# Performance work log

Measured on AMD Instinct MI355X. Metric: run time of the kernel, lower is better.

Reference implementation:

```python
import jax, jax.numpy as jnp
import numpy as np

EPS = 1e-5
B, C, T = 128, 64, 1000          # batch, EEG channels, time samples
NCLU, HID, NOUT = 8, 512, 4      # clusters, head hidden dim, outputs (=feature_dim)


def _conv1d(x, w):
    # x: (N, Cin, T), w: (Cout, Cin, K), valid conv along time
    return jax.lax.conv_general_dilated(x, w, (1,), 'VALID',
                                        dimension_numbers=('NCH', 'OIH', 'NCH'))


def _bn(x, g, b, m, v):
    # eval-mode BatchNorm over channel dim of (N, C, T)
    return (x - m[None, :, None]) * (g / jnp.sqrt(v + EPS))[None, :, None] + b[None, :, None]


def _pool3(x):
    # maxpool kernel 3 stride 3 along time
    return jax.lax.reduce_window(x, -jnp.inf, jax.lax.max, (1, 1, 3), (1, 1, 3), 'VALID')


def setup_inputs() -> dict:
    key = jax.random.key(0)
    ks = jax.random.split(key, 12)
    def nrm(k, shape, fan):
        return jax.random.normal(k, shape, jnp.float32) / np.float32(np.sqrt(fan))
    inp = {
        'x': jax.random.normal(ks[0], (B, C, T), jnp.float32),
        'cluster_ids': jax.random.randint(ks[1], (B,), 0, NCLU, jnp.int32),
        # Deep4Net-style backbone params
        'w_time': nrm(ks[2], (25, 1, 10), 10),
        'b_time': jnp.zeros((25,), jnp.float32),
        'w_spat': nrm(ks[3], (25, 25, C), 25 * C),
        'w2': nrm(ks[4], (50, 25, 10), 250),
        'w3': nrm(ks[5], (100, 50, 10), 500),
        'w4': nrm(ks[6], (200, 100, 10), 1000),
        'w_cls': nrm(ks[7], (NOUT, 200, 7), 1400),
        'b_cls': jnp.zeros((NOUT,), jnp.float32),
        # per-cluster expert head params
        'hW1': nrm(ks[8], (NCLU, HID, NOUT), NOUT),
        'hb1': jnp.zeros((NCLU, HID), jnp.float32),
        'hW2': nrm(ks[9], (NCLU, NOUT, HID), HID),
        'hb2': jnp.zeros((NCLU, NOUT), jnp.float32),
        'hg': jnp.ones((NCLU, HID), jnp.float32),
        'hbe': jnp.zeros((NCLU, HID), jnp.float32),
        'hm': jnp.zeros((NCLU, HID), jnp.float32),
        'hv': jnp.ones((NCLU, HID), jnp.float32),
    }
    for i, c in zip((1, 2, 3, 4), (25, 50, 100, 200)):
        inp[f'g{i}'] = jnp.ones((c,), jnp.float32)
        inp[f'be{i}'] = jnp.zeros((c,), jnp.float32)
        inp[f'm{i}'] = jnp.zeros((c,), jnp.float32)
        inp[f'v{i}'] = jnp.ones((c,), jnp.float32)
    return inp


def reference(x, cluster_ids, w_time, b_time, w_spat, w2, w3, w4, w_cls, b_cls,
              hW1, hb1, hW2, hb2, hg, hbe, hm, hv,
              g1, be1, m1, v1, g2, be2, m2, v2, g3, be3, m3, v3, g4, be4, m4, v4):
    b_, c_, t_ = x.shape
    # conv_time: same 25 temporal filters applied per EEG channel -> (B, C, 25, T1)
    h = _conv1d(x.reshape(b_ * c_, 1, t_), w_time) + b_time[None, :, None]
    h = h.reshape(b_, c_, 25, -1)
    # conv_spat: collapse EEG channel axis -> (B, 25, T1)
    z = jnp.einsum('bcft,gfc->bgt', h, w_spat)
    z = _pool3(jax.nn.elu(_bn(z, g1, be1, m1, v1)))
    for w, g, be, m, v in ((w2, g2, be2, m2, v2), (w3, g3, be3, m3, v3), (w4, g4, be4, m4, v4)):
        z = _pool3(jax.nn.elu(_bn(_conv1d(z, w), g, be, m, v)))
    # final_conv_length='auto': classifier conv reduces time dim to 1 -> (B, NOUT)
    feats = (_conv1d(z, w_cls) + b_cls[None, :, None])[:, :, 0]
    # per-sample expert head routing (Linear -> BN(eval) -> ReLU -> [Dropout eval] -> Linear)
    h1 = jnp.einsum('bf,bhf->bh', feats, hW1[cluster_ids]) + hb1[cluster_ids]
    h1 = (h1 - hm[cluster_ids]) * (hg[cluster_ids] / jnp.sqrt(hv[cluster_ids] + EPS)) + hbe[cluster_ids]
    h1 = jax.nn.relu(h1)
    return jnp.einsum('bh,boh->bo', h1, hW2[cluster_ids]) + hb2[cluster_ids]
```

## Files before the change

### kernel.cpp

```cpp
#include <hip/hip_runtime.h>
#include <math.h>

#define EPS_BN 1e-5f

typedef __attribute__((ext_vector_type(8))) short short8;
typedef __attribute__((ext_vector_type(4))) float f32x4;
typedef __attribute__((ext_vector_type(4))) unsigned int uint4v;

__device__ __forceinline__ unsigned short f2bf(float f) {
    unsigned int u = __float_as_uint(f);
    u = (u + 0x7fffu + ((u >> 16) & 1u)) >> 16;
    return (unsigned short)u;
}
__device__ __forceinline__ float bf2f(unsigned short s) {
    return __uint_as_float(((unsigned int)s) << 16);
}
__device__ __forceinline__ float elu1(float y) { return y > 0.f ? y : expm1f(y); }
__device__ __forceinline__ float warp_sum(float v) {
    for (int off = 32; off > 0; off >>= 1) v += __shfl_down(v, off);
    return v;
}

#define UW1 0
#define UW2 20480
#define UW3 40960
#define UW4 122880
#define BB1 0
#define BB2 32
#define BB3 96
#define BB4 224
#define XTG_U 410496
#define Z1G_U 9192320
#define Z2G_U 10544000
#define Z3G_U 11420544
#define Z4G_BYTE 24372992

#define NPREP 1602
#define RS_ZB 36

__global__ __launch_bounds__(256) void kprep_tr(
    const float* __restrict__ x,
    const float* __restrict__ w_time, const float* __restrict__ b_time,
    const float* __restrict__ w_spat,
    const float* __restrict__ w2, const float* __restrict__ w3,
    const float* __restrict__ w4,
    const float* __restrict__ g1, const float* __restrict__ be1,
    const float* __restrict__ m1, const float* __restrict__ v1,
    const float* __restrict__ g2, const float* __restrict__ be2,
    const float* __restrict__ m2, const float* __restrict__ v2,
    const float* __restrict__ g3, const float* __restrict__ be3,
    const float* __restrict__ m3, const float* __restrict__ v3,
    const float* __restrict__ g4, const float* __restrict__ be4,
    const float* __restrict__ m4, const float* __restrict__ v4,
    unsigned short* __restrict__ wsz, float* __restrict__ biasf) {
    __shared__ float tr[64 * 65];
    if (blockIdx.x < NPREP) {
        int idx = blockIdx.x * 256 + threadIdx.x;
        if (idx < 20480) {
            int k = idx >> 11, g = (idx >> 6) & 31, c = idx & 63;
            float val = 0.f;
            if (g < 25) {
                float s = 0.f;
#pragma unroll
                for (int f = 0; f < 25; ++f)
                    s = fmaf(w_spat[g * 1600 + f * 64 + c], w_time[f * 10 + k], s);
                val = s * (g1[g] * rsqrtf(v1[g] + EPS_BN));
            }
            wsz[UW1 + idx] = f2bf(val);
        } else if (idx < 40960) {
            int j = idx - 20480;
            int k = j >> 11, g = (j >> 5) & 63, c = j & 31;
            float val = 0.f;
            if (g < 50 && c < 25)
                val = w2[(g * 25 + c) * 10 + k] * (g2[g] * rsqrtf(v2[g] + EPS_BN));
            wsz[UW2 + j] = f2bf(val);
        } else if (idx < 122880) {
            int j = idx - 40960;
            int k = j >> 13, g = (j >> 6) & 127, c = j & 63;
            float val = 0.f;
            if (g < 100 && c < 50)
                val = w3[(g * 50 + c) * 10 + k] * (g3[g] * rsqrtf(v3[g] + EPS_BN));
            wsz[UW3 + j] = f2bf(val);
        } else if (idx < 409600) {
            int j = idx - 122880;
            int k = j / 28672, r = j % 28672, g = r >> 7, c = r & 127;
            float val = 0.f;
            if (g < 200 && c < 100)
                val = w4[(g * 100 + c) * 10 + k] * (g4[g] * rsqrtf(v4[g] + EPS_BN));
            wsz[UW4 + j] = f2bf(val);
        } else if (idx < 410048) {
            int j = idx - 409600;
            if (j < 32) {
                int g = j; float val = 0.f;
                if (g < 25) {
                    float beff = 0.f;
                    for (int f = 0; f < 25; ++f) {
                        float a = 0.f;
                        for (int c = 0; c < 64; ++c) a += w_spat[g * 1600 + f * 64 + c];
                        beff = fmaf(a, b_time[f], beff);
                    }
                    float sc = g1[g] * rsqrtf(v1[g] + EPS_BN);
                    val = be1[g] - m1[g] * sc + beff * sc;
                }
                biasf[BB1 + g] = val;
            } else if (j < 96) {
                int g = j - 32; float val = 0.f;
                if (g < 50) { float sc = g2[g] * rsqrtf(v2[g] + EPS_BN); val = be2[g] - m2[g] * sc; }
                biasf[BB2 + g] = val;
            } else if (j < 224) {
                int g = j - 96; float val = 0.f;
                if (g < 100) { float sc = g3[g] * rsqrtf(v3[g] + EPS_BN); val = be3[g] - m3[g] * sc; }
                biasf[BB3 + g] = val;
            } else {
                int g = j - 224; float val = 0.f;
                if (g < 200) { float sc = g4[g] * rsqrtf(v4[g] + EPS_BN); val = be4[g] - m4[g] * sc; }
                biasf[BB4 + g] = val;
            }
        }
    } else {
        const int bid = blockIdx.x - NPREP;
        const int b = bid / 17, tile = bid % 17, t = threadIdx.x;
        const int t0 = tile * 64;
        const float* xb = x + b * 64000;
        for (int idx = t; idx < 1024; idx += 256) {
            int c = idx >> 4, q = idx & 15;
            int tg = t0 + 4 * q;
            float4 v = {0.f, 0.f, 0.f, 0.f};
            if (tg + 4 <= 1000) {
                v = *(const float4*)(xb + c * 1000 + tg);
            } else {
                float* pv = (float*)&v;
#pragma unroll
                for (int e = 0; e < 4; ++e)
                    if (tg + e < 1000) pv[e] = xb[c * 1000 + tg + e];
            }
            tr[c * 65 + 4 * q]     = v.x;
            tr[c * 65 + 4 * q + 1] = v.y;
            tr[c * 65 + 4 * q + 2] = v.z;
            tr[c * 65 + 4 * q + 3] = v.w;
        }
        __syncthreads();
        unsigned short* xTg = wsz + XTG_U;
        for (int idx = t; idx < 2048; idx += 256) {
            int tl = idx >> 5, cp = idx & 31;
            int tg = t0 + tl;
            unsigned int pk = 0u;
            if (tg < 1000)
                pk = (unsigned int)f2bf(tr[(2 * cp) * 65 + tl]) |
                     ((unsigned int)f2bf(tr[(2 * cp + 1) * 65 + tl]) << 16);
            if (tg < 1072)
                *(unsigned int*)&xTg[(b * 1072 + tg) * 64 + 2 * cp] = pk;
        }
    }
}

template<int CPAD, int RS, int SP, int TT, int TPC, int NCHUNK, int JMAX,
         int NTCH, int GPAD, int TPOOL, int GSTORE, int NGV, int OUT_RS,
         bool OUT_F32, int NW, int KPRE>
__device__ __forceinline__ void conv_core(
    const unsigned short* xT, const unsigned short* __restrict__ wpk,
    const float* __restrict__ bias,
    unsigned short* zout, float* zoutf, unsigned short* zb,
    int t, int jbeg, int jend, int t0b) {
    const int lane = t & 63;
    const int wv = __builtin_amdgcn_readfirstlane(t >> 6);
    const int lm = lane & 15, h8 = lane >> 4;
    const int gloc = lane & 31, hh = lane >> 5;
    unsigned short* zbw = zb + wv * (48 * RS_ZB);

    for (int job = jbeg + wv; job < jend; job += NW) {
        const int gbi = job / NTCH, tci = job % NTCH;
        const int tl0 = tci * (TT * 16) - t0b;
        const int po0 = tci * (NCHUNK * 16);

        f32x4 acc[TT][2];
#pragma unroll
        for (int i = 0; i < TT; ++i) {
            acc[i][0] = (f32x4){0.f, 0.f, 0.f, 0.f};
            acc[i][1] = (f32x4){0.f, 0.f, 0.f, 0.f};
        }

        const int abase = (tl0 + lm) * RS + h8 * 8;
        const unsigned short* wp = wpk + (gbi * 32 + lm) * CPAD + h8 * 8;
#pragma unroll
        for (int ph = 0; ph < 10 / KPRE; ++ph) {
            short8 w0r[KPRE][SP], w1r[KPRE][SP];
#pragma unroll
            for (int kk = 0; kk < KPRE; ++kk) {
                const int k = ph * KPRE + kk;
#pragma unroll
                for (int s = 0; s < SP; ++s) {
                    w0r[kk][s] = *(const short8*)(wp + k * (GPAD * CPAD) + s * 32);
                    w1r[kk][s] = *(const short8*)(wp + k * (GPAD * CPAD) + 16 * CPAD + s * 32);
                }
            }
#pragma unroll
            for (int kk = 0; kk < KPRE; ++kk) {
                const int k = ph * KPRE + kk;
#pragma unroll
                for (int s = 0; s < SP; ++s) {
#pragma unroll
                    for (int tt = 0; tt < TT; ++tt) {
                        short8 a = *(const short8*)&xT[abase + (tt * 16 + k) * RS + s * 32];
                        acc[tt][0] = __builtin_amdgcn_mfma_f32_16x16x32_bf16(
                            a, w0r[kk][s], acc[tt][0], 0, 0, 0);
                        acc[tt][1] = __builtin_amdgcn_mfma_f32_16x16x32_bf16(
                            a, w1r[kk][s], acc[tt][1], 0, 0, 0);
                    }
                }
            }
        }

        const float bv0 = bias[gbi * 32 + lm];
        const float bv1 = bias[gbi * 32 + 16 + lm];
#pragma unroll
        for (int ch = 0; ch < NCHUNK; ++ch) {
#pragma unroll
            for (int ti = 0; ti < TPC; ++ti) {
                int ttg = ch * TPC + ti;
#pragma unroll
                for (int r = 0; r < 4; ++r) {
                    float v0 = elu1(acc[ttg][0][r] + bv0);
                    float v1 = elu1(acc[ttg][1][r] + bv1);
                    int row = ti * 16 + 4 * h8 + r;
                    zbw[row * RS_ZB + lm] = f2bf(v0);
                    zbw[row * RS_ZB + 16 + lm] = f2bf(v1);
                }
            }
#pragma unroll
            for (int j = 0; j < JMAX; ++j) {
                int po = hh + 2 * j;
                if (3 * po + 2 < TPC * 16) {
                    float q0 = bf2f(zbw[(3 * po) * RS_ZB + gloc]);
                    float q1 = bf2f(zbw[(3 * po + 1) * RS_ZB + gloc]);
                    float q2 = bf2f(zbw[(3 * po + 2) * RS_ZB + gloc]);
                    float mx = fmaxf(q0, fmaxf(q1, q2));
                    int poa = po0 + ch * 16 + po;
                    int ga = gbi * 32 + gloc;
                    if (poa < TPOOL && ga < GSTORE) {
                        if constexpr (OUT_F32)
                            zoutf[poa * OUT_RS + ga] = mx;
                        else
                            zout[poa * OUT_RS + ga] =
                                (ga < NGV) ? f2bf(mx) : (unsigned short)0;
                    }
                }
            }
        }
    }
}

__global__ __launch_bounds__(64) void ks1(
    const unsigned short* __restrict__ wsu, const float* __restrict__ biasf,
    unsigned short* __restrict__ wsz) {
    __shared__ __align__(16) unsigned short xT[64 * 72];
    __shared__ __align__(16) unsigned short zb[48 * RS_ZB];
    const int b = blockIdx.x, tci = blockIdx.y, t = threadIdx.x;
    const int t0b = tci * 48;
    const unsigned short* xTg = wsz + XTG_U + (b * 1072 + t0b) * 64;
    for (int idx = t; idx < 64 * 8; idx += 64) {
        int r = idx >> 3, q = idx & 7;
        *(uint4v*)&xT[r * 72 + 8 * q] = *(const uint4v*)&xTg[r * 64 + 8 * q];
    }
    __syncthreads();
    conv_core<64, 72, 2, 3, 3, 1, 8, 21, 32, 330, 32, 25, 32, false, 1, 5>(
        xT, wsu + UW1, biasf + BB1, wsz + Z1G_U + b * 330 * 32, nullptr, zb,
        t, tci, tci + 1, t0b);
}

__global__ __launch_bounds__(64) void ks2(
    const unsigned short* __restrict__ wsu, const float* __restrict__ biasf,
    unsigned short* __restrict__ wsz) {
    __shared__ __align__(16) unsigned short xT[64 * 40];
    __shared__ __align__(16) unsigned short zb[48 * RS_ZB];
    const int b = blockIdx.x, job = blockIdx.y, t = threadIdx.x;
    const int t0b = (job % 7) * 48;
    const unsigned short* z1g = wsz + Z1G_U + b * 330 * 32;
    for (int idx = t; idx < 64 * 4; idx += 64) {
        int r = idx >> 2, q = idx & 3;
        uint4v v = {0u, 0u, 0u, 0u};
        if (t0b + r < 330) v = *(const uint4v*)&z1g[(t0b + r) * 32 + 8 * q];
        *(uint4v*)&xT[r * 40 + 8 * q] = v;
    }
    __syncthreads();
    conv_core<32, 40, 1, 3, 3, 1, 8, 7, 64, 107, 64, 50, 64, false, 1, 5>(
        xT, wsu + UW2, biasf + BB2, wsz + Z2G_U + b * 107 * 64, nullptr, zb,
        t, job, job + 1, t0b);
}

__global__ __launch_bounds__(64) void ks3(
    const unsigned short* __restrict__ wsu, const float* __restrict__ biasf,
    unsigned short* __restrict__ wsz) {
    __shared__ __align__(16) unsigned short z2t[64 * 72];
    __shared__ __align__(16) unsigned short zb[48 * RS_ZB];
    const int b = blockIdx.x, job = blockIdx.y, t = threadIdx.x;
    const int t0b = (job % 2) * 48;
    const unsigned short* z2g = wsz + Z2G_U + b * 107 * 64;
    for (int idx = t; idx < 64 * 8; idx += 64) {
        int r = idx >> 3, q = idx & 7;
        uint4v v = {0u, 0u, 0u, 0u};
        if (t0b + r < 107) v = *(const uint4v*)&z2g[(t0b + r) * 64 + 8 * q];
        *(uint4v*)&z2t[r * 72 + 8 * q] = v;
    }
    __syncthreads();
    conv_core<64, 72, 2, 3, 3, 1, 8, 2, 128, 32, 128, 100, 136, false, 1, 5>(
        z2t, wsu + UW3, biasf + BB3, wsz + Z3G_U + b * 44 * 136, nullptr, zb,
        t, job, job + 1, t0b);
}

__global__ __launch_bounds__(64) void ks4(
    const unsigned short* __restrict__ wsu, const float* __restrict__ biasf,
    unsigned short* __restrict__ wsz, float* __restrict__ z4g) {
    __shared__ __align__(16) unsigned short z3t[44 * 136];
    __shared__ __align__(16) unsigned short zb[48 * RS_ZB];
    const int b = blockIdx.x, gbi = blockIdx.y, t = threadIdx.x;
    const unsigned short* z3g = wsz + Z3G_U + b * 44 * 136;
    for (int idx = t; idx < 44 * 17; idx += 64) {
        int r = idx / 17, q = idx % 17;
        uint4v v = {0u, 0u, 0u, 0u};
        if (r < 32) v = *(const uint4v*)&z3g[r * 136 + 8 * q];
        *(uint4v*)&z3t[r * 136 + 8 * q] = v;
    }
    __syncthreads();
    conv_core<128, 136, 4, 2, 2, 1, 4, 1, 224, 7, 200, 200, 200, true, 1, 5>(
        z3t, wsu + UW4, biasf + BB4, nullptr, z4g + b * 1400, zb,
        t, gbi, gbi + 1, 0);
}

__global__ __launch_bounds__(256) void kh(
    const float* __restrict__ z4g,
    const float* __restrict__ w_cls, const float* __restrict__ b_cls,
    const int* __restrict__ cid,
    const float* __restrict__ hW1, const float* __restrict__ hb1,
    const float* __restrict__ hW2, const float* __restrict__ hb2,
    const float* __restrict__ hg, const float* __restrict__ hbe,
    const float* __restrict__ hm, const float* __restrict__ hv,
    float* __restrict__ out) {
    __shared__ float z4f[1400];
    __shared__ float feats[4];
    __shared__ float h1s[512];
    const int b = blockIdx.x, t = threadIdx.x;
    for (int i = t; i < 1400; i += 256) z4f[i] = z4g[b * 1400 + i];
    __syncthreads();

    const int wv = t >> 6, lane = t & 63;
    {
        float p = 0.f;
        for (int i = lane; i < 1400; i += 64) {
            int po = i / 200, g = i - po * 200;
            p = fmaf(z4f[i], w_cls[wv * 1400 + g * 7 + po], p);
        }
        p = warp_sum(p);
        if (lane == 0) feats[wv] = p + b_cls[wv];
    }
    __syncthreads();

    const int c = cid[b];
    const float f0 = feats[0], f1 = feats[1], f2 = feats[2], f3 = feats[3];
    for (int h = t; h < 512; h += 256) {
        const float* w1 = &hW1[(c * 512 + h) * 4];
        float v = f0 * w1[0] + f1 * w1[1] + f2 * w1[2] + f3 * w1[3] + hb1[c * 512 + h];
        float sc = hg[c * 512 + h] * rsqrtf(hv[c * 512 + h] + EPS_BN);
        v = (v - hm[c * 512 + h]) * sc + hbe[c * 512 + h];
        h1s[h] = fmaxf(v, 0.f);
    }
    __syncthreads();
    {
        float p = 0.f;
        for (int i = lane; i < 512; i += 64)
            p = fmaf(h1s[i], hW2[(c * 4 + wv) * 512 + i], p);
        p = warp_sum(p);
        if (lane == 0) out[b * 4 + wv] = p + hb2[c * 4 + wv];
    }
}

extern "C" void kernel_launch(void* const* d_in, const int* in_sizes, int n_in,
                              void* d_out, int out_size, void* d_ws, size_t ws_size,
                              hipStream_t stream) {
    const float* x      = (const float*)d_in[0];
    const int*   cid    = (const int*)d_in[1];
    const float* w_time = (const float*)d_in[2];
    const float* b_time = (const float*)d_in[3];
    const float* w_spat = (const float*)d_in[4];
    const float* w2     = (const float*)d_in[5];
    const float* w3     = (const float*)d_in[6];
    const float* w4     = (const float*)d_in[7];
    const float* w_cls  = (const float*)d_in[8];
    const float* b_cls  = (const float*)d_in[9];
    const float* hW1    = (const float*)d_in[10];
    const float* hb1    = (const float*)d_in[11];
    const float* hW2    = (const float*)d_in[12];
    const float* hb2    = (const float*)d_in[13];
    const float* hg     = (const float*)d_in[14];
    const float* hbe    = (const float*)d_in[15];
    const float* hm     = (const float*)d_in[16];
    const float* hv     = (const float*)d_in[17];
    const float* g1  = (const float*)d_in[18];
    const float* be1 = (const float*)d_in[19];
    const float* m1  = (const float*)d_in[20];
    const float* v1  = (const float*)d_in[21];
    const float* g2  = (const float*)d_in[22];
    const float* be2 = (const float*)d_in[23];
    const float* m2  = (const float*)d_in[24];
    const float* v2  = (const float*)d_in[25];
    const float* g3  = (const float*)d_in[26];
    const float* be3 = (const float*)d_in[27];
    const float* m3  = (const float*)d_in[28];
    const float* v3  = (const float*)d_in[29];
    const float* g4  = (const float*)d_in[30];
    const float* be4 = (const float*)d_in[31];
    const float* m4  = (const float*)d_in[32];
    const float* v4  = (const float*)d_in[33];

    unsigned short* wsz = (unsigned short*)d_ws;
    float* biasf = (float*)((char*)d_ws + 819200);
    float* z4g   = (float*)((char*)d_ws + Z4G_BYTE);
    float* out = (float*)d_out;

    kprep_tr<<<NPREP + 128 * 17, 256, 0, stream>>>(
        x, w_time, b_time, w_spat, w2, w3, w4,
        g1, be1, m1, v1, g2, be2, m2, v2, g3, be3, m3, v3, g4, be4, m4, v4,
        wsz, biasf);

    ks1<<<dim3(128, 21), 64, 0, stream>>>(wsz, biasf, wsz);
    ks2<<<dim3(128, 14), 64, 0, stream>>>(wsz, biasf, wsz);
    ks3<<<dim3(128, 8), 64, 0, stream>>>(wsz, biasf, wsz);
    ks4<<<dim3(128, 7), 64, 0, stream>>>(wsz, biasf, wsz, z4g);
    kh<<<128, 256, 0, stream>>>(z4g, w_cls, b_cls, cid, hW1, hb1, hW2, hb2,
                                hg, hbe, hm, hv, out);
}
```

Baseline: 102.4 us.

## Fuse all conv stages into one persistent cooperative kernel with grid syncs

Replaces the six separate kernel launches (prep/transpose, four conv stages, head) with a single cooperative kernel of 256 blocks × 8 waves that walks each stage as a wave-level job loop separated by grid-wide barriers. Each wave stages its own input tile in a private LDS slice and uses a waitcnt fence instead of block barriers. The aim is to remove launch gaps and tail effects between the small stages. In exchange it adds grid-sync cost and fixes the parallelism at 2048 waves, which may leave some stages under-occupied or unevenly loaded.

```diff
diff --git a/kernel.cpp b/kernel.cpp
--- a/kernel.cpp
+++ b/kernel.cpp
@@ -1,5 +1,8 @@
 #include <hip/hip_runtime.h>
+#include <hip/hip_cooperative_groups.h>
 #include <math.h>
+
+namespace cg = cooperative_groups;
 
 #define EPS_BN 1e-5f
 
@@ -19,6 +22,10 @@
 __device__ __forceinline__ float warp_sum(float v) {
     for (int off = 32; off > 0; off >>= 1) v += __shfl_down(v, off);
     return v;
+}
+__device__ __forceinline__ void lds_fence() {
+    asm volatile("s_waitcnt lgkmcnt(0)" ::: "memory");
+    __builtin_amdgcn_sched_barrier(0);
 }
 
 #define UW1 0
@@ -35,27 +42,122 @@
 #define Z3G_U 11420544
 #define Z4G_BYTE 24372992
 
-#define NPREP 1602
 #define RS_ZB 36
-
-__global__ __launch_bounds__(256) void kprep_tr(
-    const float* __restrict__ x,
-    const float* __restrict__ w_time, const float* __restrict__ b_time,
-    const float* __restrict__ w_spat,
-    const float* __restrict__ w2, const float* __restrict__ w3,
-    const float* __restrict__ w4,
-    const float* __restrict__ g1, const float* __restrict__ be1,
-    const float* __restrict__ m1, const float* __restrict__ v1,
-    const float* __restrict__ g2, const float* __restrict__ be2,
-    const float* __restrict__ m2, const float* __restrict__ v2,
-    const float* __restrict__ g3, const float* __restrict__ be3,
-    const float* __restrict__ m3, const float* __restrict__ v3,
-    const float* __restrict__ g4, const float* __restrict__ be4,
-    const float* __restrict__ m4, const float* __restrict__ v4,
-    unsigned short* __restrict__ wsz, float* __restrict__ biasf) {
-    __shared__ float tr[64 * 65];
-    if (blockIdx.x < NPREP) {
-        int idx = blockIdx.x * 256 + threadIdx.x;
+#define NWAVES 2048
+#define WSCR 15424
+
+struct KParams {
+    const float* x; const int* cid;
+    const float* w_time; const float* b_time; const float* w_spat;
+    const float* w2; const float* w3; const float* w4;
+    const float* w_cls; const float* b_cls;
+    const float* hW1; const float* hb1; const float* hW2; const float* hb2;
+    const float* hg; const float* hbe; const float* hm; const float* hv;
+    const float* g1; const float* be1; const float* m1; const float* v1;
+    const float* g2; const float* be2; const float* m2; const float* v2;
+    const float* g3; const float* be3; const float* m3; const float* v3;
+    const float* g4; const float* be4; const float* m4; const float* v4;
+    unsigned short* wsz; float* biasf; float* z4g; float* out;
+};
+
+template<int CPAD, int RS, int SP, int TT, int TPC, int NCHUNK, int JMAX,
+         int GPAD, int TPOOL, int GSTORE, int NGV, int OUT_RS, bool OUT_F32,
+         int KPRE>
+__device__ __forceinline__ void conv_job(
+    const unsigned short* xT, const unsigned short* __restrict__ wpk,
+    const float* __restrict__ bias,
+    unsigned short* zout, float* zoutf, unsigned short* zbw,
+    int lane, int gbi, int po0) {
+    const int lm = lane & 15, h8 = lane >> 4;
+    const int gloc = lane & 31, hh = lane >> 5;
+
+    f32x4 acc[TT][2];
+#pragma unroll
+    for (int i = 0; i < TT; ++i) {
+        acc[i][0] = (f32x4){0.f, 0.f, 0.f, 0.f};
+        acc[i][1] = (f32x4){0.f, 0.f, 0.f, 0.f};
+    }
+
+    const int abase = lm * RS + h8 * 8;
+    const unsigned short* wp = wpk + (gbi * 32 + lm) * CPAD + h8 * 8;
+#pragma unroll
+    for (int ph = 0; ph < 10 / KPRE; ++ph) {
+        short8 w0r[KPRE][SP], w1r[KPRE][SP];
+#pragma unroll
+        for (int kk = 0; kk < KPRE; ++kk) {
+            const int k = ph * KPRE + kk;
+#pragma unroll
+            for (int s = 0; s < SP; ++s) {
+                w0r[kk][s] = *(const short8*)(wp + k * (GPAD * CPAD) + s * 32);
+                w1r[kk][s] = *(const short8*)(wp + k * (GPAD * CPAD) + 16 * CPAD + s * 32);
+            }
+        }
+#pragma unroll
+        for (int kk = 0; kk < KPRE; ++kk) {
+            const int k = ph * KPRE + kk;
+#pragma unroll
+            for (int s = 0; s < SP; ++s) {
+#pragma unroll
+                for (int tt = 0; tt < TT; ++tt) {
+                    short8 a = *(const short8*)&xT[abase + (tt * 16 + k) * RS + s * 32];
+                    acc[tt][0] = __builtin_amdgcn_mfma_f32_16x16x32_bf16(
+                        a, w0r[kk][s], acc[tt][0], 0, 0, 0);
+                    acc[tt][1] = __builtin_amdgcn_mfma_f32_16x16x32_bf16(
+                        a, w1r[kk][s], acc[tt][1], 0, 0, 0);
+                }
+            }
+        }
+    }
+
+    const float bv0 = bias[gbi * 32 + lm];
+    const float bv1 = bias[gbi * 32 + 16 + lm];
+#pragma unroll
+    for (int ch = 0; ch < NCHUNK; ++ch) {
+#pragma unroll
+        for (int ti = 0; ti < TPC; ++ti) {
+            int ttg = ch * TPC + ti;
+#pragma unroll
+            for (int r = 0; r < 4; ++r) {
+                float v0 = elu1(acc[ttg][0][r] + bv0);
+                float v1 = elu1(acc[ttg][1][r] + bv1);
+                int row = ti * 16 + 4 * h8 + r;
+                zbw[row * RS_ZB + lm] = f2bf(v0);
+                zbw[row * RS_ZB + 16 + lm] = f2bf(v1);
+            }
+        }
+#pragma unroll
+        for (int j = 0; j < JMAX; ++j) {
+            int po = hh + 2 * j;
+            if (3 * po + 2 < TPC * 16) {
+                float q0 = bf2f(zbw[(3 * po) * RS_ZB + gloc]);
+                float q1 = bf2f(zbw[(3 * po + 1) * RS_ZB + gloc]);
+                float q2 = bf2f(zbw[(3 * po + 2) * RS_ZB + gloc]);
+                float mx = fmaxf(q0, fmaxf(q1, q2));
+                int poa = po0 + ch * 16 + po;
+                int ga = gbi * 32 + gloc;
+                if (poa < TPOOL && ga < GSTORE) {
+                    if constexpr (OUT_F32)
+                        zoutf[poa * OUT_RS + ga] = mx;
+                    else
+                        zout[poa * OUT_RS + ga] =
+                            (ga < NGV) ? f2bf(mx) : (unsigned short)0;
+                }
+            }
+        }
+    }
+}
+
+__global__ __launch_bounds__(512, 2) void kfused(KParams P) {
+    __shared__ __align__(16) unsigned char smem[8 * WSCR];
+    const int t = threadIdx.x;
+    const int lane = t & 63;
+    const int wv = t >> 6;
+    const int W = blockIdx.x * 8 + wv;
+    unsigned short* tile = (unsigned short*)(smem + wv * WSCR);
+    unsigned short* zbw  = (unsigned short*)(smem + wv * WSCR + 11968);
+    cg::grid_group gg = cg::this_grid();
+
+    for (int idx = blockIdx.x * 512 + t; idx < 410048; idx += 131072) {
         if (idx < 20480) {
             int k = idx >> 11, g = (idx >> 6) & 31, c = idx & 63;
             float val = 0.f;
@@ -63,31 +165,31 @@
                 float s = 0.f;
 #pragma unroll
                 for (int f = 0; f < 25; ++f)
-                    s = fmaf(w_spat[g * 1600 + f * 64 + c], w_time[f * 10 + k], s);
-                val = s * (g1[g] * rsqrtf(v1[g] + EPS_BN));
-            }
-            wsz[UW1 + idx] = f2bf(val);
+                    s = fmaf(P.w_spat[g * 1600 + f * 64 + c], P.w_time[f * 10 + k], s);
+                val = s * (P.g1[g] * rsqrtf(P.v1[g] + EPS_BN));
+            }
+            P.wsz[UW1 + idx] = f2bf(val);
         } else if (idx < 40960) {
             int j = idx - 20480;
             int k = j >> 11, g = (j >> 5) & 63, c = j & 31;
             float val = 0.f;
             if (g < 50 && c < 25)
-                val = w2[(g * 25 + c) * 10 + k] * (g2[g] * rsqrtf(v2[g] + EPS_BN));
-            wsz[UW2 + j] = f2bf(val);
+                val = P.w2[(g * 25 + c) * 10 + k] * (P.g2[g] * rsqrtf(P.v2[g] + EPS_BN));
+            P.wsz[UW2 + j] = f2bf(val);
         } else if (idx < 122880) {
             int j = idx - 40960;
             int k = j >> 13, g = (j >> 6) & 127, c = j & 63;
             float val = 0.f;
             if (g < 100 && c < 50)
-                val = w3[(g * 50 + c) * 10 + k] * (g3[g] * rsqrtf(v3[g] + EPS_BN));
-            wsz[UW3 + j] = f2bf(val);
+                val = P.w3[(g * 50 + c) * 10 + k] * (P.g3[g] * rsqrtf(P.v3[g] + EPS_BN));
+            P.wsz[UW3 + j] = f2bf(val);
         } else if (idx < 409600) {
             int j = idx - 122880;
             int k = j / 28672, r = j % 28672, g = r >> 7, c = r & 127;
             float val = 0.f;
             if (g < 200 && c < 100)
-                val = w4[(g * 100 + c) * 10 + k] * (g4[g] * rsqrtf(v4[g] + EPS_BN));
-            wsz[UW4 + j] = f2bf(val);
+                val = P.w4[(g * 100 + c) * 10 + k] * (P.g4[g] * rsqrtf(P.v4[g] + EPS_BN));
+            P.wsz[UW4 + j] = f2bf(val);
         } else if (idx < 410048) {
             int j = idx - 409600;
             if (j < 32) {
@@ -96,336 +198,214 @@
                     float beff = 0.f;
                     for (int f = 0; f < 25; ++f) {
                         float a = 0.f;
-                        for (int c = 0; c < 64; ++c) a += w_spat[g * 1600 + f * 64 + c];
-                        beff = fmaf(a, b_time[f], beff);
+                        for (int c = 0; c < 64; ++c) a += P.w_spat[g * 1600 + f * 64 + c];
+                        beff = fmaf(a, P.b_time[f], beff);
                     }
-                    float sc = g1[g] * rsqrtf(v1[g] + EPS_BN);
-                    val = be1[g] - m1[g] * sc + beff * sc;
+                    float sc = P.g1[g] * rsqrtf(P.v1[g] + EPS_BN);
+                    val = P.be1[g] - P.m1[g] * sc + beff * sc;
                 }
-                biasf[BB1 + g] = val;
+                P.biasf[BB1 + g] = val;
             } else if (j < 96) {
                 int g = j - 32; float val = 0.f;
-                if (g < 50) { float sc = g2[g] * rsqrtf(v2[g] + EPS_BN); val = be2[g] - m2[g] * sc; }
-                biasf[BB2 + g] = val;
+                if (g < 50) { float sc = P.g2[g] * rsqrtf(P.v2[g] + EPS_BN); val = P.be2[g] - P.m2[g] * sc; }
+                P.biasf[BB2 + g] = val;
             } else if (j < 224) {
                 int g = j - 96; float val = 0.f;
-                if (g < 100) { float sc = g3[g] * rsqrtf(v3[g] + EPS_BN); val = be3[g] - m3[g] * sc; }
-                biasf[BB3 + g] = val;
+                if (g < 100) { float sc = P.g3[g] * rsqrtf(P.v3[g] + EPS_BN); val = P.be3[g] - P.m3[g] * sc; }
+                P.biasf[BB3 + g] = val;
             } else {
                 int g = j - 224; float val = 0.f;
-                if (g < 200) { float sc = g4[g] * rsqrtf(v4[g] + EPS_BN); val = be4[g] - m4[g] * sc; }
-                biasf[BB4 + g] = val;
-            }
-        }
-    } else {
-        const int bid = blockIdx.x - NPREP;
-        const int b = bid / 17, tile = bid % 17, t = threadIdx.x;
-        const int t0 = tile * 64;
-        const float* xb = x + b * 64000;
-        for (int idx = t; idx < 1024; idx += 256) {
-            int c = idx >> 4, q = idx & 15;
-            int tg = t0 + 4 * q;
-            float4 v = {0.f, 0.f, 0.f, 0.f};
-            if (tg + 4 <= 1000) {
-                v = *(const float4*)(xb + c * 1000 + tg);
-            } else {
-                float* pv = (float*)&v;
-#pragma unroll
-                for (int e = 0; e < 4; ++e)
-                    if (tg + e < 1000) pv[e] = xb[c * 1000 + tg + e];
-            }
-            tr[c * 65 + 4 * q]     = v.x;
-            tr[c * 65 + 4 * q + 1] = v.y;
-            tr[c * 65 + 4 * q + 2] = v.z;
-            tr[c * 65 + 4 * q + 3] = v.w;
-        }
+                if (g < 200) { float sc = P.g4[g] * rsqrtf(P.v4[g] + EPS_BN); val = P.be4[g] - P.m4[g] * sc; }
+                P.biasf[BB4 + g] = val;
+            }
+        }
+    }
+
+    {
+        float* tr = (float*)smem;
+        unsigned short* xTg = P.wsz + XTG_U;
+        for (int tid2 = blockIdx.x; tid2 < 2176; tid2 += 256) {
+            const int b = tid2 / 17, tilei = tid2 % 17;
+            const int t0 = tilei * 64;
+            const float* xb = P.x + b * 64000;
+            __syncthreads();
+            for (int idx = t; idx < 1024; idx += 512) {
+                int c = idx >> 4, q = idx & 15;
+                int tg = t0 + 4 * q;
+                float4 v = {0.f, 0.f, 0.f, 0.f};
+                if (tg + 4 <= 1000) {
+                    v = *(const float4*)(xb + c * 1000 + tg);
+                } else {
+                    float* pv = (float*)&v;
+#pragma unroll
+                    for (int e = 0; e < 4; ++e)
+                        if (tg + e < 1000) pv[e] = xb[c * 1000 + tg + e];
+                }
+                tr[c * 65 + 4 * q]     = v.x;
+                tr[c * 65 + 4 * q + 1] = v.y;
+                tr[c * 65 + 4 * q + 2] = v.z;
+                tr[c * 65 + 4 * q + 3] = v.w;
+            }
+            __syncthreads();
+            for (int idx = t; idx < 2048; idx += 512) {
+                int tl = idx >> 5, cp = idx & 31;
+                int tg = t0 + tl;
+                unsigned int pk = 0u;
+                if (tg < 1000)
+                    pk = (unsigned int)f2bf(tr[(2 * cp) * 65 + tl]) |
+                         ((unsigned int)f2bf(tr[(2 * cp + 1) * 65 + tl]) << 16);
+                if (tg < 1072)
+                    *(unsigned int*)&xTg[(b * 1072 + tg) * 64 + 2 * cp] = pk;
+            }
+        }
+    }
+    gg.sync();
+
+    for (int jid = W; jid < 2688; jid += NWAVES) {
+        const int b = jid / 21, tci = jid % 21;
+        const unsigned short* src = P.wsz + XTG_U + (b * 1072 + tci * 48) * 64;
+        for (int idx = lane; idx < 512; idx += 64) {
+            int r = idx >> 3, q = idx & 7;
+            *(uint4v*)&tile[r * 72 + 8 * q] = *(const uint4v*)&src[r * 64 + 8 * q];
+        }
+        lds_fence();
+        conv_job<64, 72, 2, 3, 3, 1, 8, 32, 330, 32, 25, 32, false, 5>(
+            tile, P.wsz + UW1, P.biasf + BB1,
+            P.wsz + Z1G_U + b * 330 * 32, nullptr, zbw, lane, 0, tci * 16);
+    }
+    gg.sync();
+
+    for (int jid = W; jid < 1792; jid += NWAVES) {
+        const int b = jid / 14, y = jid % 14;
+        const int gbi = y / 7, tci = y % 7, t0b = tci * 48;
+        const unsigned short* z1g = P.wsz + Z1G_U + b * 330 * 32;
+        for (int idx = lane; idx < 256; idx += 64) {
+            int r = idx >> 2, q = idx & 3;
+            uint4v v = {0u, 0u, 0u, 0u};
+            if (t0b + r < 330) v = *(const uint4v*)&z1g[(t0b + r) * 32 + 8 * q];
+            *(uint4v*)&tile[r * 40 + 8 * q] = v;
+        }
+        lds_fence();
+        conv_job<32, 40, 1, 3, 3, 1, 8, 64, 107, 64, 50, 64, false, 5>(
+            tile, P.wsz + UW2, P.biasf + BB2,
+            P.wsz + Z2G_U + b * 107 * 64, nullptr, zbw, lane, gbi, tci * 16);
+    }
+    gg.sync();
+
+    for (int jid = W; jid < 1024; jid += NWAVES) {
+        const int b = jid / 8, y = jid % 8;
+        const int gbi = y / 2, tci = y % 2, t0b = tci * 48;
+        const unsigned short* z2g = P.wsz + Z2G_U + b * 107 * 64;
+        for (int idx = lane; idx < 512; idx += 64) {
+            int r = idx >> 3, q = idx & 7;
+            uint4v v = {0u, 0u, 0u, 0u};
+            if (t0b + r < 107) v = *(const uint4v*)&z2g[(t0b + r) * 64 + 8 * q];
+            *(uint4v*)&tile[r * 72 + 8 * q] = v;
+        }
+        lds_fence();
+        conv_job<64, 72, 2, 3, 3, 1, 8, 128, 32, 128, 100, 136, false, 5>(
+            tile, P.wsz + UW3, P.biasf + BB3,
+            P.wsz + Z3G_U + b * 44 * 136, nullptr, zbw, lane, gbi, tci * 16);
+    }
+    gg.sync();
+
+    for (int jid = W; jid < 896; jid += NWAVES) {
+        const int b = jid / 7, gbi = jid % 7;
+        const unsigned short* z3g = P.wsz + Z3G_U + b * 44 * 136;
+        for (int idx = lane; idx < 748; idx += 64) {
+            int r = idx / 17, q = idx % 17;
+            uint4v v = {0u, 0u, 0u, 0u};
+            if (r < 32) v = *(const uint4v*)&z3g[r * 136 + 8 * q];
+            *(uint4v*)&tile[r * 136 + 8 * q] = v;
+        }
+        lds_fence();
+        conv_job<128, 136, 4, 2, 2, 1, 4, 224, 7, 200, 200, 200, true, 5>(
+            tile, P.wsz + UW4, P.biasf + BB4,
+            nullptr, P.z4g + b * 1400, zbw, lane, gbi, 0);
+    }
+    gg.sync();
+
+    if (blockIdx.x < 128) {
+        const int b = blockIdx.x;
+        float* z4f   = (float*)smem;
+        float* feats = (float*)(smem + 5600);
+        float* h1s   = (float*)(smem + 5616);
+        for (int i = t; i < 1400; i += 512) z4f[i] = P.z4g[b * 1400 + i];
         __syncthreads();
-        unsigned short* xTg = wsz + XTG_U;
-        for (int idx = t; idx < 2048; idx += 256) {
-            int tl = idx >> 5, cp = idx & 31;
-            int tg = t0 + tl;
-            unsigned int pk = 0u;
-            if (tg < 1000)
-                pk = (unsigned int)f2bf(tr[(2 * cp) * 65 + tl]) |
-                     ((unsigned int)f2bf(tr[(2 * cp + 1) * 65 + tl]) << 16);
-            if (tg < 1072)
-                *(unsigned int*)&xTg[(b * 1072 + tg) * 64 + 2 * cp] = pk;
-        }
-    }
-}
-
-template<int CPAD, int RS, int SP, int TT, int TPC, int NCHUNK, int JMAX,
-         int NTCH, int GPAD, int TPOOL, int GSTORE, int NGV, int OUT_RS,
-         bool OUT_F32, int NW, int KPRE>
-__device__ __forceinline__ void conv_core(
-    const unsigned short* xT, const unsigned short* __restrict__ wpk,
-    const float* __restrict__ bias,
-    unsigned short* zout, float* zoutf, unsigned short* zb,
-    int t, int jbeg, int jend, int t0b) {
-    const int lane = t & 63;
-    const int wv = __builtin_amdgcn_readfirstlane(t >> 6);
-    const int lm = lane & 15, h8 = lane >> 4;
-    const int gloc = lane & 31, hh = lane >> 5;
-    unsigned short* zbw = zb + wv * (48 * RS_ZB);
-
-    for (int job = jbeg + wv; job < jend; job += NW) {
-        const int gbi = job / NTCH, tci = job % NTCH;
-        const int tl0 = tci * (TT * 16) - t0b;
-        const int po0 = tci * (NCHUNK * 16);
-
-        f32x4 acc[TT][2];
-#pragma unroll
-        for (int i = 0; i < TT; ++i) {
-            acc[i][0] = (f32x4){0.f, 0.f, 0.f, 0.f};
-            acc[i][1] = (f32x4){0.f, 0.f, 0.f, 0.f};
-        }
-
-        const int abase = (tl0 + lm) * RS + h8 * 8;
-        const unsigned short* wp = wpk + (gbi * 32 + lm) * CPAD + h8 * 8;
-#pragma unroll
-        for (int ph = 0; ph < 10 / KPRE; ++ph) {
-            short8 w0r[KPRE][SP], w1r[KPRE][SP];
-#pragma unroll
-            for (int kk = 0; kk < KPRE; ++kk) {
-                const int k = ph * KPRE + kk;
-#pragma unroll
-                for (int s = 0; s < SP; ++s) {
-                    w0r[kk][s] = *(const short8*)(wp + k * (GPAD * CPAD) + s * 32);
-                    w1r[kk][s] = *(const short8*)(wp + k * (GPAD * CPAD) + 16 * CPAD + s * 32);
-                }
-            }
-#pragma unroll
-            for (int kk = 0; kk < KPRE; ++kk) {
-                const int k = ph * KPRE + kk;
-#pragma unroll
-                for (int s = 0; s < SP; ++s) {
-#pragma unroll
-                    for (int tt = 0; tt < TT; ++tt) {
-                        short8 a = *(const short8*)&xT[abase + (tt * 16 + k) * RS + s * 32];
-                        acc[tt][0] = __builtin_amdgcn_mfma_f32_16x16x32_bf16(
-                            a, w0r[kk][s], acc[tt][0], 0, 0, 0);
-                        acc[tt][1] = __builtin_amdgcn_mfma_f32_16x16x32_bf16(
-                            a, w1r[kk][s], acc[tt][1], 0, 0, 0);
-                    }
-                }
-            }
-        }
-
-        const float bv0 = bias[gbi * 32 + lm];
-        const float bv1 = bias[gbi * 32 + 16 + lm];
-#pragma unroll
-        for (int ch = 0; ch < NCHUNK; ++ch) {
-#pragma unroll
-            for (int ti = 0; ti < TPC; ++ti) {
-                int ttg = ch * TPC + ti;
-#pragma unroll
-                for (int r = 0; r < 4; ++r) {
-                    float v0 = elu1(acc[ttg][0][r] + bv0);
-                    float v1 = elu1(acc[ttg][1][r] + bv1);
-                    int row = ti * 16 + 4 * h8 + r;
-                    zbw[row * RS_ZB + lm] = f2bf(v0);
-                    zbw[row * RS_ZB + 16 + lm] = f2bf(v1);
-                }
-            }
-#pragma unroll
-            for (int j = 0; j < JMAX; ++j) {
-                int po = hh + 2 * j;
-                if (3 * po + 2 < TPC * 16) {
-                    float q0 = bf2f(zbw[(3 * po) * RS_ZB + gloc]);
-                    float q1 = bf2f(zbw[(3 * po + 1) * RS_ZB + gloc]);
-                    float q2 = bf2f(zbw[(3 * po + 2) * RS_ZB + gloc]);
-                    float mx = fmaxf(q0, fmaxf(q1, q2));
-                    int poa = po0 + ch * 16 + po;
-                    int ga = gbi * 32 + gloc;
-                    if (poa < TPOOL && ga < GSTORE) {
-                        if constexpr (OUT_F32)
-                            zoutf[poa * OUT_RS + ga] = mx;
-                        else
-                            zout[poa * OUT_RS + ga] =
-                                (ga < NGV) ? f2bf(mx) : (unsigned short)0;
-                    }
-                }
-            }
-        }
-    }
-}
-
-__global__ __launch_bounds__(64) void ks1(
-    const unsigned short* __restrict__ wsu, const float* __restrict__ biasf,
-    unsigned short* __restrict__ wsz) {
-    __shared__ __align__(16) unsigned short xT[64 * 72];
-    __shared__ __align__(16) unsigned short zb[48 * RS_ZB];
-    const int b = blockIdx.x, tci = blockIdx.y, t = threadIdx.x;
-    const int t0b = tci * 48;
-    const unsigned short* xTg = wsz + XTG_U + (b * 1072 + t0b) * 64;
-    for (int idx = t; idx < 64 * 8; idx += 64) {
-        int r = idx >> 3, q = idx & 7;
-        *(uint4v*)&xT[r * 72 + 8 * q] = *(const uint4v*)&xTg[r * 64 + 8 * q];
-    }
-    __syncthreads();
-    conv_core<64, 72, 2, 3, 3, 1, 8, 21, 32, 330, 32, 25, 32, false, 1, 5>(
-        xT, wsu + UW1, biasf + BB1, wsz + Z1G_U + b * 330 * 32, nullptr, zb,
-        t, tci, tci + 1, t0b);
-}
-
-__global__ __launch_bounds__(64) void ks2(
-    const unsigned short* __restrict__ wsu, const float* __restrict__ biasf,
-    unsigned short* __restrict__ wsz) {
-    __shared__ __align__(16) unsigned short xT[64 * 40];
-    __shared__ __align__(16) unsigned short zb[48 * RS_ZB];
-    const int b = blockIdx.x, job = blockIdx.y, t = threadIdx.x;
-    const int t0b = (job % 7) * 48;
-    const unsigned short* z1g = wsz + Z1G_U + b * 330 * 32;
-    for (int idx = t; idx < 64 * 4; idx += 64) {
-        int r = idx >> 2, q = idx & 3;
-        uint4v v = {0u, 0u, 0u, 0u};
-        if (t0b + r < 330) v = *(const uint4v*)&z1g[(t0b + r) * 32 + 8 * q];
-        *(uint4v*)&xT[r * 40 + 8 * q] = v;
-    }
-    __syncthreads();
-    conv_core<32, 40, 1, 3, 3, 1, 8, 7, 64, 107, 64, 50, 64, false, 1, 5>(
-        xT, wsu + UW2, biasf + BB2, wsz + Z2G_U + b * 107 * 64, nullptr, zb,
-        t, job, job + 1, t0b);
-}
-
-__global__ __launch_bounds__(64) void ks3(
-    const unsigned short* __restrict__ wsu, const float* __restrict__ biasf,
-    unsigned short* __restrict__ wsz) {
-    __shared__ __align__(16) unsigned short z2t[64 * 72];
-    __shared__ __align__(16) unsigned short zb[48 * RS_ZB];
-    const int b = blockIdx.x, job = blockIdx.y, t = threadIdx.x;
-    const int t0b = (job % 2) * 48;
-    const unsigned short* z2g = wsz + Z2G_U + b * 107 * 64;
-    for (int idx = t; idx < 64 * 8; idx += 64) {
-        int r = idx >> 3, q = idx & 7;
-        uint4v v = {0u, 0u, 0u, 0u};
-        if (t0b + r < 107) v = *(const uint4v*)&z2g[(t0b + r) * 64 + 8 * q];
-        *(uint4v*)&z2t[r * 72 + 8 * q] = v;
-    }
-    __syncthreads();
-    conv_core<64, 72, 2, 3, 3, 1, 8, 2, 128, 32, 128, 100, 136, false, 1, 5>(
-        z2t, wsu + UW3, biasf + BB3, wsz + Z3G_U + b * 44 * 136, nullptr, zb,
-        t, job, job + 1, t0b);
-}
-
-__global__ __launch_bounds__(64) void ks4(
-    const unsigned short* __restrict__ wsu, const float* __restrict__ biasf,
-    unsigned short* __restrict__ wsz, float* __restrict__ z4g) {
-    __shared__ __align__(16) unsigned short z3t[44 * 136];
-    __shared__ __align__(16) unsigned short zb[48 * RS_ZB];
-    const int b = blockIdx.x, gbi = blockIdx.y, t = threadIdx.x;
-    const unsigned short* z3g = wsz + Z3G_U + b * 44 * 136;
-    for (int idx = t; idx < 44 * 17; idx += 64) {
-        int r = idx / 17, q = idx % 17;
-        uint4v v = {0u, 0u, 0u, 0u};
-        if (r < 32) v = *(const uint4v*)&z3g[r * 136 + 8 * q];
-        *(uint4v*)&z3t[r * 136 + 8 * q] = v;
-    }
-    __syncthreads();
-    conv_core<128, 136, 4, 2, 2, 1, 4, 1, 224, 7, 200, 200, 200, true, 1, 5>(
-        z3t, wsu + UW4, biasf + BB4, nullptr, z4g + b * 1400, zb,
-        t, gbi, gbi + 1, 0);
-}
-
-__global__ __launch_bounds__(256) void kh(
-    const float* __restrict__ z4g,
-    const float* __restrict__ w_cls, const float* __restrict__ b_cls,
-    const int* __restrict__ cid,
-    const float* __restrict__ hW1, const float* __restrict__ hb1,
-    const float* __restrict__ hW2, const float* __restrict__ hb2,
-    const float* __restrict__ hg, const float* __restrict__ hbe,
-    const float* __restrict__ hm, const float* __restrict__ hv,
-    float* __restrict__ out) {
-    __shared__ float z4f[1400];
-    __shared__ float feats[4];
-    __shared__ float h1s[512];
-    const int b = blockIdx.x, t = threadIdx.x;
-    for (int i = t; i < 1400; i += 256) z4f[i] = z4g[b * 1400 + i];
-    __syncthreads();
-
-    const int wv = t >> 6, lane = t & 63;
-    {
-        float p = 0.f;
-        for (int i = lane; i < 1400; i += 64) {
-            int po = i / 200, g = i - po * 200;
-            p = fmaf(z4f[i], w_cls[wv * 1400 + g * 7 + po], p);
-        }
-        p = warp_sum(p);
-        if (lane == 0) feats[wv] = p + b_cls[wv];
-    }
-    __syncthreads();
-
-    const int c = cid[b];
-    const float f0 = feats[0], f1 = feats[1], f2 = feats[2], f3 = feats[3];
-    for (int h = t; h < 512; h += 256) {
-        const float* w1 = &hW1[(c * 512 + h) * 4];
-        float v = f0 * w1[0] + f1 * w1[1] + f2 * w1[2] + f3 * w1[3] + hb1[c * 512 + h];
-        float sc = hg[c * 512 + h] * rsqrtf(hv[c * 512 + h] + EPS_BN);
-        v = (v - hm[c * 512 + h]) * sc + hbe[c * 512 + h];
-        h1s[h] = fmaxf(v, 0.f);
-    }
-    __syncthreads();
-    {
-        float p = 0.f;
-        for (int i = lane; i < 512; i += 64)
-            p = fmaf(h1s[i], hW2[(c * 4 + wv) * 512 + i], p);
-        p = warp_sum(p);
-        if (lane == 0) out[b * 4 + wv] = p + hb2[c * 4 + wv];
+        if (wv < 4) {
+            float p = 0.f;
+            for (int i = lane; i < 1400; i += 64) {
+                int po = i / 200, g = i - po * 200;
+                p = fmaf(z4f[i], P.w_cls[wv * 1400 + g * 7 + po], p);
+            }
+            p = warp_sum(p);
+            if (lane == 0) feats[wv] = p + P.b_cls[wv];
+        }
+        __syncthreads();
+        const int c = P.cid[b];
+        const float f0 = feats[0], f1 = feats[1], f2 = feats[2], f3 = feats[3];
+        for (int h = t; h < 512; h += 512) {
+            const float* w1 = &P.hW1[(c * 512 + h) * 4];
+            float v = f0 * w1[0] + f1 * w1[1] + f2 * w1[2] + f3 * w1[3] + P.hb1[c * 512 + h];
+            float sc = P.hg[c * 512 + h] * rsqrtf(P.hv[c * 512 + h] + EPS_BN);
+            v = (v - P.hm[c * 512 + h]) * sc + P.hbe[c * 512 + h];
+            h1s[h] = fmaxf(v, 0.f);
+        }
+        __syncthreads();
+        if (wv < 4) {
+            float p = 0.f;
+            for (int i = lane; i < 512; i += 64)
+                p = fmaf(h1s[i], P.hW2[(c * 4 + wv) * 512 + i], p);
+            p = warp_sum(p);
+            if (lane == 0) P.out[b * 4 + wv] = p + P.hb2[c * 4 + wv];
+        }
     }
 }
 
 extern "C" void kernel_launch(void* const* d_in, const int* in_sizes, int n_in,
                               void* d_out, int out_size, void* d_ws, size_t ws_size,
                               hipStream_t stream) {
-    const float* x      = (const float*)d_in[0];
-    const int*   cid    = (const int*)d_in[1];
-    const float* w_time = (const float*)d_in[2];
-    const float* b_time = (const float*)d_in[3];
-    const float* w_spat = (const float*)d_in[4];
-    const float* w2     = (const float*)d_in[5];
-    const float* w3     = (const float*)d_in[6];
-    const float* w4     = (const float*)d_in[7];
-    const float* w_cls  = (const float*)d_in[8];
-    const float* b_cls  = (const float*)d_in[9];
-    const float* hW1    = (const float*)d_in[10];
-    const float* hb1    = (const float*)d_in[11];
-    const float* hW2    = (const float*)d_in[12];
-    const float* hb2    = (const float*)d_in[13];
-    const float* hg     = (const float*)d_in[14];
-    const float* hbe    = (const float*)d_in[15];
-    const float* hm     = (const float*)d_in[16];
-    const float* hv     = (const float*)d_in[17];
-    const float* g1  = (const float*)d_in[18];
-    const float* be1 = (const float*)d_in[19];
-    const float* m1  = (const float*)d_in[20];
-    const float* v1  = (const float*)d_in[21];
-    const float* g2  = (const float*)d_in[22];
-    const float* be2 = (const float*)d_in[23];
-    const float* m2  = (const float*)d_in[24];
-    const float* v2  = (const float*)d_in[25];
-    const float* g3  = (const float*)d_in[26];
-    const float* be3 = (const float*)d_in[27];
-    const float* m3  = (const float*)d_in[28];
-    const float* v3  = (const float*)d_in[29];
-    const float* g4  = (const float*)d_in[30];
-    const float* be4 = (const float*)d_in[31];
-    const float* m4  = (const float*)d_in[32];
-    const float* v4  = (const float*)d_in[33];
-
-    unsigned short* wsz = (unsigned short*)d_ws;
-    float* biasf = (float*)((char*)d_ws + 819200);
-    float* z4g   = (float*)((char*)d_ws + Z4G_BYTE);
-    float* out = (float*)d_out;
-
-    kprep_tr<<<NPREP + 128 * 17, 256, 0, stream>>>(
-        x, w_time, b_time, w_spat, w2, w3, w4,
-        g1, be1, m1, v1, g2, be2, m2, v2, g3, be3, m3, v3, g4, be4, m4, v4,
-        wsz, biasf);
-
-    ks1<<<dim3(128, 21), 64, 0, stream>>>(wsz, biasf, wsz);
-    ks2<<<dim3(128, 14), 64, 0, stream>>>(wsz, biasf, wsz);
-    ks3<<<dim3(128, 8), 64, 0, stream>>>(wsz, biasf, wsz);
-    ks4<<<dim3(128, 7), 64, 0, stream>>>(wsz, biasf, wsz, z4g);
-    kh<<<128, 256, 0, stream>>>(z4g, w_cls, b_cls, cid, hW1, hb1, hW2, hb2,
-                                hg, hbe, hm, hv, out);
-}
+    KParams P;
+    P.x      = (const float*)d_in[0];
+    P.cid    = (const int*)d_in[1];
+    P.w_time = (const float*)d_in[2];
+    P.b_time = (const float*)d_in[3];
+    P.w_spat = (const float*)d_in[4];
+    P.w2     = (const float*)d_in[5];
+    P.w3     = (const float*)d_in[6];
+    P.w4     = (const float*)d_in[7];
+    P.w_cls  = (const float*)d_in[8];
+    P.b_cls  = (const float*)d_in[9];
+    P.hW1    = (const float*)d_in[10];
+    P.hb1    = (const float*)d_in[11];
+    P.hW2    = (const float*)d_in[12];
+    P.hb2    = (const float*)d_in[13];
+    P.hg     = (const float*)d_in[14];
+    P.hbe    = (const float*)d_in[15];
+    P.hm     = (const float*)d_in[16];
+    P.hv     = (const float*)d_in[17];
+    P.g1  = (const float*)d_in[18];
+    P.be1 = (const float*)d_in[19];
+    P.m1  = (const float*)d_in[20];
+    P.v1  = (const float*)d_in[21];
+    P.g2  = (const float*)d_in[22];
+    P.be2 = (const float*)d_in[23];
+    P.m2  = (const float*)d_in[24];
+    P.v2  = (const float*)d_in[25];
+    P.g3  = (const float*)d_in[26];
+    P.be3 = (const float*)d_in[27];
+    P.m3  = (const float*)d_in[28];
+    P.v3  = (const float*)d_in[29];
+    P.g4  = (const float*)d_in[30];
+    P.be4 = (const float*)d_in[31];
+    P.m4  = (const float*)d_in[32];
+    P.v4  = (const float*)d_in[33];
+    P.wsz   = (unsigned short*)d_ws;
+    P.biasf = (float*)((char*)d_ws + 819200);
+    P.z4g   = (float*)((char*)d_ws + Z4G_BYTE);
+    P.out   = (float*)d_out;
+
+    void* kargs[] = {(void*)&P};
+    hipLaunchCooperativeKernel((const void*)kfused, dim3(256), dim3(512),
+                               kargs, 0, stream);
+}
```

Result: slower. 276.0 us (+169.4%).
